# Performance work log

Measured on AMD Instinct MI355X. Metric: run time of the kernel, lower is better.

## Reference

```python
import jax, jax.numpy as jnp
import numpy as np

B, C, H, Wd = 16, 512, 56, 56
WCH = 128  # W_ch: projection rank of phi/rou


def setup_inputs() -> dict:
    key = jax.random.key(0)
    ks = jax.random.split(key, 8)
    s = 0.02
    return {
        "x": jax.random.normal(ks[0], (B, C, H, Wd), dtype=jnp.float32),
        "y": jax.random.normal(ks[1], (B, C, H, Wd), dtype=jnp.float32),
        # phi: Conv2d(C, WCH, 1) -> weight [WCH, C], bias [WCH]
        "phi_w": jax.random.normal(ks[2], (WCH, C), dtype=jnp.float32) * s,
        "phi_b": jnp.zeros((WCH,), dtype=jnp.float32),
        # rou: Conv2d(C, WCH, 1) applied to globally pooled y -> acts as Linear
        "rou_w": jax.random.normal(ks[3], (WCH, C), dtype=jnp.float32) * s,
        "rou_b": jnp.zeros((WCH,), dtype=jnp.float32),
        # zeta: Linear(C, C)
        "zeta_w": jax.random.normal(ks[4], (C, C), dtype=jnp.float32) * s,
        "zeta_b": jnp.zeros((C,), dtype=jnp.float32),
    }


def reference(x, y, phi_w, phi_b, rou_w, rou_b, zeta_w, zeta_b):
    b, c, h, w = x.shape
    hw = h * w
    # phi_xT = relu(phi(x)).view(B, WCH, HW); phi_x = transpose -> [B, HW, WCH]
    phi_xT = jax.nn.relu(jnp.einsum('kc,bchw->bkhw', phi_w, x) + phi_b[None, :, None, None])
    phi_x = phi_xT.reshape(b, -1, hw).transpose(0, 2, 1)  # [B, HW, WCH]
    # rou_y = sigmoid(rou(global_avg_pool(y))) -> [B, WCH]
    pooled = y.mean(axis=(2, 3))  # [B, C]
    rou_y = jax.nn.sigmoid(pooled @ rou_w.T + rou_b)  # [B, WCH]
    # D_i = sum_j (phi_x diag(rou) phi_x^T)_{ij} = sum_k phi_x[i,k] rou[k] s[k]
    s = phi_x.sum(axis=1)  # [B, WCH], column sums
    D = jnp.einsum('bnk,bk,bk->bn', phi_x, rou_y, s)  # [B, HW]
    inv_sqrt = 1.0 / jnp.sqrt(D + 1e-8)
    P = phi_x * inv_sqrt[..., None]  # diag(D^-1/2) @ phi_x, [B, HW, WCH]
    # x.view(B, -1, C): raw row-major reshape of [B,C,H,W] (NOT a transpose)
    x_trans = x.reshape(b, hw, c)
    # LX = x_trans - P diag(rou) P^T x_trans, re-associated right-to-left
    t = jnp.einsum('bnk,bnc->bkc', P, x_trans)          # P^T x_trans, [B, WCH, C]
    LX = x_trans - jnp.einsum('bnk,bk,bkc->bnc', P, rou_y, t)
    # zeta Linear + dropout(eval: identity) + relu, residual add
    out = jax.nn.relu(LX @ zeta_w.T + zeta_b)
    return x + out.reshape(b, c, h, w)
```

## Files before the change

### kernel.cpp

```cpp
#include <hip/hip_runtime.h>
#include <math.h>

#define B_  16
#define C_  512
#define HW_ 3136
#define K_  128
#define CHW (C_ * HW_)

typedef __bf16 bf16x8_t __attribute__((ext_vector_type(8)));
typedef __bf16 bf16x4_t __attribute__((ext_vector_type(4)));
typedef __bf16 bf16x2_t __attribute__((ext_vector_type(2)));
typedef float floatx4  __attribute__((ext_vector_type(4)));

typedef const __attribute__((address_space(1))) void* gas_ptr;
typedef __attribute__((address_space(3))) void*       las_ptr;

__device__ __forceinline__ void stage128x64(const __bf16* __restrict__ base, long ld,
                                            int row0, int rowmax, int k0,
                                            __bf16* lds, int t) {
    int w = t >> 6;
    #pragma unroll
    for (int i = 0; i < 4; ++i) {
        int u = i * 256 + t;
        int m = u >> 3, slot = u & 7;
        int kg = slot ^ (m & 7);
        int r = row0 + m; if (r > rowmax) r = rowmax;
        const __bf16* g = base + (long)r * ld + (k0 + kg * 8);
        __bf16* l = lds + (size_t)(i * 256 + w * 64) * 8;
        __builtin_amdgcn_global_load_lds((gas_ptr)g, (las_ptr)l, 16, 0, 0);
    }
}

__device__ __forceinline__ void mma_step64(const char* As, const char* Bs,
                                           floatx4 acc[4][4], int aoff, int boff,
                                           int q, int lxor) {
    #pragma unroll
    for (int h = 0; h < 2; ++h) {
        int s = (((h * 4 + q) ^ lxor) << 4);
        bf16x8_t af[4], bf[4];
        #pragma unroll
        for (int i = 0; i < 4; ++i)
            af[i] = *(const bf16x8_t*)(As + aoff + i * 2048 + s);
        #pragma unroll
        for (int i = 0; i < 4; ++i)
            bf[i] = *(const bf16x8_t*)(Bs + boff + i * 2048 + s);
        #pragma unroll
        for (int mi = 0; mi < 4; ++mi)
            #pragma unroll
            for (int ni = 0; ni < 4; ++ni)
                acc[mi][ni] = __builtin_amdgcn_mfma_f32_16x16x32_bf16(af[mi], bf[ni], acc[mi][ni], 0, 0, 0);
    }
}


__global__ __launch_bounds__(256) void k_pool(const float* __restrict__ y,
                                              float* __restrict__ pooled) {
    int bc = blockIdx.x;
    const float* yp = y + (long)bc * HW_;
    float acc = 0.f;
    for (int n = threadIdx.x; n < HW_; n += 256) acc += yp[n];
    __shared__ float red[256];
    red[threadIdx.x] = acc;
    __syncthreads();
    for (int s = 128; s > 0; s >>= 1) {
        if (threadIdx.x < s) red[threadIdx.x] += red[threadIdx.x + s];
        __syncthreads();
    }
    if (threadIdx.x == 0) pooled[bc] = red[0] * (1.0f / HW_);
}

__global__ __launch_bounds__(128) void k_rou(const float* __restrict__ pooled,
                                             const float* __restrict__ rou_w,
                                             const float* __restrict__ rou_b,
                                             float* __restrict__ rou_y) {
    int b = blockIdx.x;
    int k = threadIdx.x;
    __shared__ float ps[C_];
    for (int c = threadIdx.x; c < C_; c += 128) ps[c] = pooled[b * C_ + c];
    __syncthreads();
    float acc = rou_b[k];
    for (int c = 0; c < C_; ++c) acc += ps[c] * rou_w[k * C_ + c];
    rou_y[b * K_ + k] = 1.0f / (1.0f + expf(-acc));
}

__global__ __launch_bounds__(256) void k_cast8(const float* __restrict__ a,
                                               __bf16* __restrict__ o) {
    long i = ((long)blockIdx.x * 256 + threadIdx.x) * 8;
    float4 v0 = *reinterpret_cast<const float4*>(a + i);
    float4 v1 = *reinterpret_cast<const float4*>(a + i + 4);
    bf16x8_t r;
    r[0] = (__bf16)v0.x; r[1] = (__bf16)v0.y; r[2] = (__bf16)v0.z; r[3] = (__bf16)v0.w;
    r[4] = (__bf16)v1.x; r[5] = (__bf16)v1.y; r[6] = (__bf16)v1.z; r[7] = (__bf16)v1.w;
    *reinterpret_cast<bf16x8_t*>(o + i) = r;
}

__global__ __launch_bounds__(256) void k_prep(const float* __restrict__ xf,
                                              __bf16* __restrict__ xbf2,
                                              __bf16* __restrict__ x1t) {
    int b = blockIdx.z, c0 = blockIdx.y * 64, n0 = blockIdx.x * 64;
    __shared__ float ld[64][65];
    int t = threadIdx.x, tn = t & 63, g = t >> 6;
    const float* xb = xf + (long)b * CHW;
    __bf16* fb = xbf2 + (long)b * CHW;
    #pragma unroll 4
    for (int r = 0; r < 16; ++r) {
        int c = c0 + g * 16 + r;
        float v = xb[(long)c * HW_ + n0 + tn];
        ld[g * 16 + r][tn] = v;
        fb[(long)c * HW_ + n0 + tn] = (__bf16)v;
    }
    __syncthreads();
    __bf16* ob = x1t + (long)b * CHW;
    #pragma unroll 4
    for (int r = 0; r < 16; ++r) {
        int n = n0 + g * 16 + r;
        ob[(long)n * C_ + c0 + tn] = (__bf16)ld[tn][g * 16 + r];
    }
}

__global__ __launch_bounds__(256) void k_tr2s(const __bf16* __restrict__ xbf2,
                                              const float* __restrict__ inv_s,
                                              __bf16* __restrict__ x2s) {
    int b = blockIdx.z, c0 = blockIdx.y * 64, n0 = blockIdx.x * 64;
    __shared__ float ld[64][65];
    int t = threadIdx.x, tc = t & 63, g = t >> 6;
    const __bf16* xb = xbf2 + (long)b * CHW;
    #pragma unroll 4
    for (int r = 0; r < 16; ++r) {
        int n = n0 + g * 16 + r;
        ld[g * 16 + r][tc] = (float)xb[(long)n * C_ + c0 + tc] * inv_s[b * HW_ + n];
    }
    __syncthreads();
    __bf16* ob = x2s + (long)b * CHW;
    #pragma unroll 4
    for (int r = 0; r < 16; ++r) {
        int c = c0 + g * 16 + r;
        ob[(long)c * HW_ + n0 + tc] = (__bf16)ld[tc][g * 16 + r];
    }
}


__global__ __launch_bounds__(256) void k_phi_m(const __bf16* __restrict__ x1t,
                                               const __bf16* __restrict__ pwbf,
                                               const float* __restrict__ phi_b,
                                               __bf16* __restrict__ phi_kn,
                                               __bf16* __restrict__ phi_nk,
                                               float* __restrict__ sbuf) {
    int b = blockIdx.y;
    int n0 = blockIdx.x * 128;
    __shared__ __bf16 As[8192];
    __shared__ __bf16 Bs[8192];
    int t = threadIdx.x, w = t >> 6, lane = t & 63;
    int lm = lane & 15, q = lane >> 4;
    int wrow = w >> 1, wcol = w & 1;
    floatx4 acc[4][4];
    #pragma unroll
    for (int i = 0; i < 4; ++i)
        #pragma unroll
        for (int j = 0; j < 4; ++j) acc[i][j] = (floatx4){0.f, 0.f, 0.f, 0.f};

    const __bf16* Bb = x1t + (long)b * CHW;
    int lxor = lm & 7;
    int aoff = (wrow * 64 + lm) * 128;
    int boff = (wcol * 64 + lm) * 128;

    for (int p0 = 0; p0 < C_; p0 += 64) {
        stage128x64(pwbf, C_, 0, K_ - 1, p0, As, t);
        stage128x64(Bb,   C_, n0, HW_ - 1, p0, Bs, t);
        __syncthreads();
        mma_step64((const char*)As, (const char*)Bs, acc, aoff, boff, q, lxor);
        __syncthreads();
    }
    #pragma unroll
    for (int mi = 0; mi < 4; ++mi) {
        int kb = wrow * 64 + mi * 16 + q * 4;
        float4 pb = *reinterpret_cast<const float4*>(phi_b + kb);
        float pbv[4] = {pb.x, pb.y, pb.z, pb.w};
        float sv[4] = {0.f, 0.f, 0.f, 0.f};
        #pragma unroll
        for (int ni = 0; ni < 4; ++ni) {
            int n = n0 + wcol * 64 + ni * 16 + lm;
            if (n < HW_) {
                bf16x4_t pack;
                #pragma unroll
                for (int r = 0; r < 4; ++r) {
                    float v = fmaxf(acc[mi][ni][r] + pbv[r], 0.f);
                    __bf16 vb = (__bf16)v;
                    phi_kn[((long)b * K_ + kb + r) * HW_ + n] = vb;
                    pack[r] = vb;
                    sv[r] += v;
                }
                *reinterpret_cast<bf16x4_t*>(phi_nk + ((long)b * HW_ + n) * K_ + kb) = pack;
            }
        }
        #pragma unroll
        for (int r = 0; r < 4; ++r) {
            float v = sv[r];
            v += __shfl_xor(v, 1, 64); v += __shfl_xor(v, 2, 64);
            v += __shfl_xor(v, 4, 64); v += __shfl_xor(v, 8, 64);
            if (lm == 0) atomicAdd(&sbuf[b * K_ + kb + r], v);
        }
    }
}

__global__ __launch_bounds__(256) void k_d2(__bf16* __restrict__ phi_nk,
                                            const float* __restrict__ rou_y,
                                            const float* __restrict__ s,
                                            float* __restrict__ inv_s) {
    int b = blockIdx.y;
    __shared__ float ws[K_];
    int t = threadIdx.x;
    if (t < K_) ws[t] = rou_y[b * K_ + t] * s[b * K_ + t];
    __syncthreads();
    int w = t >> 6, lane = t & 63;
    int n = blockIdx.x * 4 + w;
    __bf16* p = phi_nk + ((long)b * HW_ + n) * K_ + lane * 2;
    bf16x2_t v = *reinterpret_cast<bf16x2_t*>(p);
    float f0 = (float)v[0], f1 = (float)v[1];
    float d = f0 * ws[lane * 2] + f1 * ws[lane * 2 + 1];
    #pragma unroll
    for (int off = 32; off > 0; off >>= 1) d += __shfl_xor(d, off, 64);
    float inv = rsqrtf(d + 1e-8f);
    bf16x2_t o; o[0] = (__bf16)(f0 * inv); o[1] = (__bf16)(f1 * inv);
    *reinterpret_cast<bf16x2_t*>(p) = o;
    if (lane == 0) inv_s[b * HW_ + n] = inv;
}

__global__ __launch_bounds__(256) void k_t_m(const __bf16* __restrict__ phi_kn,
                                             const __bf16* __restrict__ x2s,
                                             float* __restrict__ t_f32) {
    int b = blockIdx.z;
    int c0 = blockIdx.x * 128;
    int nch = blockIdx.y;
    __shared__ __bf16 As[8192];
    __shared__ __bf16 Bs[8192];
    int t = threadIdx.x, w = t >> 6, lane = t & 63;
    int lm = lane & 15, q = lane >> 4;
    int wrow = w >> 1, wcol = w & 1;
    floatx4 acc[4][4];
    #pragma unroll
    for (int i = 0; i < 4; ++i)
        #pragma unroll
        for (int j = 0; j < 4; ++j) acc[i][j] = (floatx4){0.f, 0.f, 0.f, 0.f};

    const __bf16* Ab = phi_kn + (long)b * K_ * HW_;
    const __bf16* Bb = x2s + (long)b * CHW;
    int lxor = lm & 7;
    int aoff = (wrow * 64 + lm) * 128;
    int boff = (wcol * 64 + lm) * 128;

    int pstart = nch * 448;
    for (int p0 = pstart; p0 < pstart + 448; p0 += 64) {
        stage128x64(Ab, HW_, 0, K_ - 1, p0, As, t);
        stage128x64(Bb, HW_, c0, C_ - 1, p0, Bs, t);
        __syncthreads();
        mma_step64((const char*)As, (const char*)Bs, acc, aoff, boff, q, lxor);
        __syncthreads();
    }
    #pragma unroll
    for (int mi = 0; mi < 4; ++mi) {
        int kb = wrow * 64 + mi * 16 + q * 4;
        #pragma unroll
        for (int ni = 0; ni < 4; ++ni) {
            int c = c0 + wcol * 64 + ni * 16 + lm;
            #pragma unroll
            for (int r = 0; r < 4; ++r)
                atomicAdd(&t_f32[((long)b * K_ + kb + r) * C_ + c], acc[mi][ni][r]);
        }
    }
}

__global__ __launch_bounds__(256) void k_tz_m(const __bf16* __restrict__ zwbf,
                                              const __bf16* __restrict__ t_bf,
                                              const float* __restrict__ rou_y,
                                              __bf16* __restrict__ tzT) {
    int b = blockIdx.y;
    int c0 = blockIdx.x * 128;
    __shared__ __bf16 As[8192];
    __shared__ __bf16 Bs[8192];
    int t = threadIdx.x, w = t >> 6, lane = t & 63;
    int lm = lane & 15, q = lane >> 4;
    int wrow = w >> 1, wcol = w & 1;
    floatx4 acc[4][4];
    #pragma unroll
    for (int i = 0; i < 4; ++i)
        #pragma unroll
        for (int j = 0; j < 4; ++j) acc[i][j] = (floatx4){0.f, 0.f, 0.f, 0.f};

    const __bf16* Bb = t_bf + (long)b * K_ * C_;
    int lxor = lm & 7;
    int aoff = (wrow * 64 + lm) * 128;
    int boff = (wcol * 64 + lm) * 128;

    for (int p0 = 0; p0 < C_; p0 += 64) {
        stage128x64(zwbf, C_, c0, C_ - 1, p0, As, t);
        stage128x64(Bb,   C_, 0, K_ - 1, p0, Bs, t);
        __syncthreads();
        mma_step64((const char*)As, (const char*)Bs, acc, aoff, boff, q, lxor);
        __syncthreads();
    }
    #pragma unroll
    for (int mi = 0; mi < 4; ++mi) {
        int c = c0 + wrow * 64 + mi * 16 + q * 4;
        #pragma unroll
        for (int ni = 0; ni < 4; ++ni) {
            int k = wcol * 64 + ni * 16 + lm;
            float rk = rou_y[b * K_ + k];
            #pragma unroll
            for (int r = 0; r < 4; ++r)
                tzT[((long)b * C_ + c + r) * K_ + k] = (__bf16)(-rk * acc[mi][ni][r]);
        }
    }
}

__global__ __launch_bounds__(256) void k_out_m(const __bf16* __restrict__ xbf2,
                                               const __bf16* __restrict__ zwbf,
                                               const __bf16* __restrict__ pnk,
                                               const __bf16* __restrict__ tzT,
                                               const float* __restrict__ zeta_b,
                                               float* __restrict__ out) {
    int b = blockIdx.z;
    int n0 = blockIdx.y * 128;
    int c0 = blockIdx.x * 128;
    __shared__ __attribute__((aligned(16))) char smem[32768];
    __bf16* As = (__bf16*)smem;
    __bf16* Bs = (__bf16*)(smem + 16384);
    int t = threadIdx.x, w = t >> 6, lane = t & 63;
    int lm = lane & 15, q = lane >> 4;
    int wrow = w >> 1, wcol = w & 1;
    floatx4 acc[4][4];
    #pragma unroll
    for (int i = 0; i < 4; ++i)
        #pragma unroll
        for (int j = 0; j < 4; ++j) acc[i][j] = (floatx4){0.f, 0.f, 0.f, 0.f};

    int lxor = lm & 7;
    int aoff = (wrow * 64 + lm) * 128;
    int boff = (wcol * 64 + lm) * 128;

    const __bf16* A1 = xbf2 + (long)b * CHW;
    for (int p0 = 0; p0 < C_; p0 += 64) {
        stage128x64(A1,   C_, n0, HW_ - 1, p0, As, t);
        stage128x64(zwbf, C_, c0, C_ - 1, p0, Bs, t);
        __syncthreads();
        mma_step64((const char*)As, (const char*)Bs, acc, aoff, boff, q, lxor);
        __syncthreads();
    }
    const __bf16* A2 = pnk + (long)b * (long)HW_ * K_;
    const __bf16* B2 = tzT + (long)b * (long)C_ * K_;
    for (int p0 = 0; p0 < K_; p0 += 64) {
        stage128x64(A2, K_, n0, HW_ - 1, p0, As, t);
        stage128x64(B2, K_, c0, C_ - 1, p0, Bs, t);
        __syncthreads();
        mma_step64((const char*)As, (const char*)Bs, acc, aoff, boff, q, lxor);
        __syncthreads();
    }
    float* ep = (float*)smem;
    const __bf16* xres = xbf2 + (long)b * CHW;
    int lr = t >> 3, lc = (t & 7) * 16;
    #pragma unroll
    for (int ch = 0; ch < 4; ++ch) {
        __syncthreads();
        if (wrow == (ch >> 1)) {
            #pragma unroll
            for (int mm = 0; mm < 2; ++mm) {
                int mi = (ch & 1) * 2 + mm;
                #pragma unroll
                for (int ni = 0; ni < 4; ++ni)
                    #pragma unroll
                    for (int r = 0; r < 4; ++r)
                        ep[(mm * 16 + q * 4 + r) * 132 + wcol * 64 + ni * 16 + lm] = acc[mi][ni][r];
            }
        }
        __syncthreads();
        int n = n0 + ch * 32 + lr;
        if (n < HW_) {
            long rowbase = (long)n * C_ + c0 + lc;
            bf16x8_t x0 = *(const bf16x8_t*)(xres + rowbase);
            bf16x8_t x1 = *(const bf16x8_t*)(xres + rowbase + 8);
            float xv[16];
            #pragma unroll
            for (int j = 0; j < 8; ++j) { xv[j] = (float)x0[j]; xv[8 + j] = (float)x1[j]; }
            float* orow = out + (long)b * CHW + rowbase;
            #pragma unroll
            for (int jj = 0; jj < 4; ++jj) {
                float4 zb = *reinterpret_cast<const float4*>(zeta_b + c0 + lc + jj * 4);
                float4 e  = *reinterpret_cast<const float4*>(&ep[lr * 132 + lc + jj * 4]);
                float4 o;
                o.x = xv[jj * 4 + 0] + fmaxf(e.x + zb.x, 0.f);
                o.y = xv[jj * 4 + 1] + fmaxf(e.y + zb.y, 0.f);
                o.z = xv[jj * 4 + 2] + fmaxf(e.z + zb.z, 0.f);
                o.w = xv[jj * 4 + 3] + fmaxf(e.w + zb.w, 0.f);
                *reinterpret_cast<float4*>(orow + jj * 4) = o;
            }
        }
    }
}

extern "C" void kernel_launch(void* const* d_in, const int* in_sizes, int n_in,
                              void* d_out, int out_size, void* d_ws, size_t ws_size,
                              hipStream_t stream) {
    const float* x      = (const float*)d_in[0];
    const float* y      = (const float*)d_in[1];
    const float* phi_w  = (const float*)d_in[2];
    const float* phi_b  = (const float*)d_in[3];
    const float* rou_w  = (const float*)d_in[4];
    const float* rou_b  = (const float*)d_in[5];
    const float* zeta_w = (const float*)d_in[6];
    const float* zeta_b = (const float*)d_in[7];
    float* out = (float*)d_out;

    char* p = (char*)d_ws;
    __bf16* xbf2   = (__bf16*)p; p += (size_t)B_ * CHW * 2;
    __bf16* x1t    = (__bf16*)p; p += (size_t)B_ * CHW * 2;
    __bf16* phi_kn = (__bf16*)p; p += (size_t)B_ * K_ * HW_ * 2;
    __bf16* phi_nk = (__bf16*)p; p += (size_t)B_ * K_ * HW_ * 2;
    float*  t_f32  = (float*) p; p += (size_t)B_ * K_ * C_ * 4;
    __bf16* tzT    = (__bf16*)p; p += (size_t)B_ * C_ * K_ * 2;
    __bf16* pwbf   = (__bf16*)p; p += (size_t)K_ * C_ * 2;
    __bf16* zwbf   = (__bf16*)p; p += (size_t)C_ * C_ * 2;
    float*  pooled = (float*) p; p += (size_t)B_ * C_ * 4;
    float*  rou_y  = (float*) p; p += (size_t)B_ * K_ * 4;
    float*  sbuf   = (float*) p; p += (size_t)B_ * K_ * 4;
    float*  inv_s  = (float*) p; p += (size_t)B_ * HW_ * 4;
    __bf16* x2s    = x1t;
    __bf16* t_bf   = x1t;

    hipMemsetAsync(sbuf, 0, B_ * K_ * sizeof(float), stream);
    hipMemsetAsync(t_f32, 0, (size_t)B_ * K_ * C_ * sizeof(float), stream);

    k_pool <<<B_ * C_, 256, 0, stream>>>(y, pooled);
    k_rou  <<<B_, 128, 0, stream>>>(pooled, rou_w, rou_b, rou_y);
    k_cast8<<<(K_ * C_) / 2048, 256, 0, stream>>>(phi_w, pwbf);
    k_cast8<<<(C_ * C_) / 2048, 256, 0, stream>>>(zeta_w, zwbf);
    k_prep <<<dim3(HW_ / 64, C_ / 64, B_), 256, 0, stream>>>(x, xbf2, x1t);
    k_phi_m<<<dim3(25, B_), 256, 0, stream>>>(x1t, pwbf, phi_b, phi_kn, phi_nk, sbuf);
    k_d2   <<<dim3(HW_ / 4, B_), 256, 0, stream>>>(phi_nk, rou_y, sbuf, inv_s);
    k_tr2s <<<dim3(HW_ / 64, C_ / 64, B_), 256, 0, stream>>>(xbf2, inv_s, x2s);
    k_t_m  <<<dim3(C_ / 128, 7, B_), 256, 0, stream>>>(phi_kn, x2s, t_f32);
    k_cast8<<<(B_ * K_ * C_) / 2048, 256, 0, stream>>>(t_f32, t_bf);
    k_tz_m <<<dim3(C_ / 128, B_), 256, 0, stream>>>(zwbf, t_bf, rou_y, tzT);
    k_out_m<<<dim3(C_ / 128, 25, B_), 256, 0, stream>>>(xbf2, zwbf, phi_nk, tzT, zeta_b, out);
}
```

Baseline: 476.3 us.

## Fuse transposes into GEMM staging and replace atomic split-K with partial reduction

Removes the separate transpose kernels (k_prep, k_tr2s). The phi and t GEMMs now read the raw bf16 copy of x and transpose it in-register while staging into a padded, swizzled LDS tile, with the inv_sqrt scaling folded into the t staging. Split-K atomics into t_f32, along with its memset, are replaced by per-chunk partial buffers reduced by a new kernel that also does the bf16 cast. Block indices of the t and out GEMMs are remapped to a 1D grid, which changes the order in which tiles are scheduled. This saves full-tensor transpose traffic and atomics, at the cost of synchronous global loads in place of async global_load_lds for the B operand, plus extra workspace for the partials.

```diff
diff --git a/kernel.cpp b/kernel.cpp
--- a/kernel.cpp
+++ b/kernel.cpp
@@ -14,6 +14,10 @@
 
 typedef const __attribute__((address_space(1))) void* gas_ptr;
 typedef __attribute__((address_space(3))) void*       las_ptr;
+
+static __device__ __forceinline__ unsigned short bfbits(__bf16 v) {
+    return __builtin_bit_cast(unsigned short, v);
+}
 
 __device__ __forceinline__ void stage128x64(const __bf16* __restrict__ base, long ld,
                                             int row0, int rowmax, int k0,
@@ -31,6 +35,53 @@
     }
 }
 
+__device__ __forceinline__ void stage_tr_phi(const __bf16* __restrict__ src,
+                                             int n0, int p0, char* Bs, int t) {
+    int ng = t & 15;
+    int cp2 = (t >> 4) * 2;
+    #pragma unroll
+    for (int ci = 0; ci < 2; ++ci) {
+        int cc = cp2 + ci * 32;
+        const __bf16* g0 = src + (long)(p0 + cc) * HW_ + n0 + ng * 8;
+        bf16x8_t v0 = *(const bf16x8_t*)g0;
+        bf16x8_t v1 = *(const bf16x8_t*)(g0 + HW_);
+        int r8 = cc >> 3, sub = (cc & 7) >> 1;
+        #pragma unroll
+        for (int j = 0; j < 8; ++j) {
+            int row = ng * 8 + j;
+            int slot = (r8 + row + (row >> 3)) & 7;
+            unsigned int pr = ((unsigned int)bfbits(v1[j]) << 16) | bfbits(v0[j]);
+            *(unsigned int*)(Bs + row * 144 + slot * 16 + sub * 4) = pr;
+        }
+    }
+}
+
+__device__ __forceinline__ void stage_tr_t(const __bf16* __restrict__ src,
+                                           const float* __restrict__ isrc,
+                                           int c0, int p0, char* Bs, int t) {
+    int cg = t & 15;
+    int np2 = (t >> 4) * 2;
+    #pragma unroll
+    for (int ni = 0; ni < 2; ++ni) {
+        int nn = np2 + ni * 32;
+        int n = p0 + nn;
+        float s0 = isrc[n], s1 = isrc[n + 1];
+        const __bf16* g0 = src + (long)n * C_ + c0 + cg * 8;
+        bf16x8_t v0 = *(const bf16x8_t*)g0;
+        bf16x8_t v1 = *(const bf16x8_t*)(g0 + C_);
+        int r8 = nn >> 3, sub = (nn & 7) >> 1;
+        #pragma unroll
+        for (int j = 0; j < 8; ++j) {
+            int row = cg * 8 + j;
+            int slot = (r8 + row + (row >> 3)) & 7;
+            __bf16 a0 = (__bf16)((float)v0[j] * s0);
+            __bf16 a1 = (__bf16)((float)v1[j] * s1);
+            unsigned int pr = ((unsigned int)bfbits(a1) << 16) | bfbits(a0);
+            *(unsigned int*)(Bs + row * 144 + slot * 16 + sub * 4) = pr;
+        }
+    }
+}
+
 __device__ __forceinline__ void mma_step64(const char* As, const char* Bs,
                                            floatx4 acc[4][4], int aoff, int boff,
                                            int q, int lxor) {
@@ -39,11 +90,35 @@
         int s = (((h * 4 + q) ^ lxor) << 4);
         bf16x8_t af[4], bf[4];
         #pragma unroll
-        for (int i = 0; i < 4; ++i)
-            af[i] = *(const bf16x8_t*)(As + aoff + i * 2048 + s);
-        #pragma unroll
-        for (int i = 0; i < 4; ++i)
-            bf[i] = *(const bf16x8_t*)(Bs + boff + i * 2048 + s);
+        for (int i = 0; i < 4; ++i) af[i] = *(const bf16x8_t*)(As + aoff + i * 2048 + s);
+        #pragma unroll
+        for (int i = 0; i < 4; ++i) bf[i] = *(const bf16x8_t*)(Bs + boff + i * 2048 + s);
+        #pragma unroll
+        for (int mi = 0; mi < 4; ++mi)
+            #pragma unroll
+            for (int ni = 0; ni < 4; ++ni)
+                acc[mi][ni] = __builtin_amdgcn_mfma_f32_16x16x32_bf16(af[mi], bf[ni], acc[mi][ni], 0, 0, 0);
+    }
+}
+
+__device__ __forceinline__ void mma_step_mix(const char* As, const char* Bs,
+                                             floatx4 acc[4][4], int lm, int q,
+                                             int wrow, int wcol) {
+    int lxor = lm & 7;
+    int aoff = (wrow * 64 + lm) * 128;
+    #pragma unroll
+    for (int h = 0; h < 2; ++h) {
+        int g = h * 4 + q;
+        int sa = (g ^ lxor) << 4;
+        bf16x8_t af[4], bf[4];
+        #pragma unroll
+        for (int i = 0; i < 4; ++i) af[i] = *(const bf16x8_t*)(As + aoff + i * 2048 + sa);
+        #pragma unroll
+        for (int i = 0; i < 4; ++i) {
+            int brow = wcol * 64 + i * 16 + lm;
+            int slot = (g + brow + (brow >> 3)) & 7;
+            bf[i] = *(const bf16x8_t*)(Bs + brow * 144 + slot * 16);
+        }
         #pragma unroll
         for (int mi = 0; mi < 4; ++mi)
             #pragma unroll
@@ -94,53 +169,8 @@
     *reinterpret_cast<bf16x8_t*>(o + i) = r;
 }
 
-__global__ __launch_bounds__(256) void k_prep(const float* __restrict__ xf,
-                                              __bf16* __restrict__ xbf2,
-                                              __bf16* __restrict__ x1t) {
-    int b = blockIdx.z, c0 = blockIdx.y * 64, n0 = blockIdx.x * 64;
-    __shared__ float ld[64][65];
-    int t = threadIdx.x, tn = t & 63, g = t >> 6;
-    const float* xb = xf + (long)b * CHW;
-    __bf16* fb = xbf2 + (long)b * CHW;
-    #pragma unroll 4
-    for (int r = 0; r < 16; ++r) {
-        int c = c0 + g * 16 + r;
-        float v = xb[(long)c * HW_ + n0 + tn];
-        ld[g * 16 + r][tn] = v;
-        fb[(long)c * HW_ + n0 + tn] = (__bf16)v;
-    }
-    __syncthreads();
-    __bf16* ob = x1t + (long)b * CHW;
-    #pragma unroll 4
-    for (int r = 0; r < 16; ++r) {
-        int n = n0 + g * 16 + r;
-        ob[(long)n * C_ + c0 + tn] = (__bf16)ld[tn][g * 16 + r];
-    }
-}
-
-__global__ __launch_bounds__(256) void k_tr2s(const __bf16* __restrict__ xbf2,
-                                              const float* __restrict__ inv_s,
-                                              __bf16* __restrict__ x2s) {
-    int b = blockIdx.z, c0 = blockIdx.y * 64, n0 = blockIdx.x * 64;
-    __shared__ float ld[64][65];
-    int t = threadIdx.x, tc = t & 63, g = t >> 6;
-    const __bf16* xb = xbf2 + (long)b * CHW;
-    #pragma unroll 4
-    for (int r = 0; r < 16; ++r) {
-        int n = n0 + g * 16 + r;
-        ld[g * 16 + r][tc] = (float)xb[(long)n * C_ + c0 + tc] * inv_s[b * HW_ + n];
-    }
-    __syncthreads();
-    __bf16* ob = x2s + (long)b * CHW;
-    #pragma unroll 4
-    for (int r = 0; r < 16; ++r) {
-        int c = c0 + g * 16 + r;
-        ob[(long)c * HW_ + n0 + tc] = (__bf16)ld[tc][g * 16 + r];
-    }
-}
-
-
-__global__ __launch_bounds__(256) void k_phi_m(const __bf16* __restrict__ x1t,
+
+__global__ __launch_bounds__(256) void k_phi_m(const __bf16* __restrict__ xbf2,
                                                const __bf16* __restrict__ pwbf,
                                                const float* __restrict__ phi_b,
                                                __bf16* __restrict__ phi_kn,
@@ -148,8 +178,8 @@
                                                float* __restrict__ sbuf) {
     int b = blockIdx.y;
     int n0 = blockIdx.x * 128;
-    __shared__ __bf16 As[8192];
-    __shared__ __bf16 Bs[8192];
+    __shared__ __attribute__((aligned(16))) char smem[16384 + 18432];
+    char* As = smem; char* Bs = smem + 16384;
     int t = threadIdx.x, w = t >> 6, lane = t & 63;
     int lm = lane & 15, q = lane >> 4;
     int wrow = w >> 1, wcol = w & 1;
@@ -159,16 +189,12 @@
         #pragma unroll
         for (int j = 0; j < 4; ++j) acc[i][j] = (floatx4){0.f, 0.f, 0.f, 0.f};
 
-    const __bf16* Bb = x1t + (long)b * CHW;
-    int lxor = lm & 7;
-    int aoff = (wrow * 64 + lm) * 128;
-    int boff = (wcol * 64 + lm) * 128;
-
+    const __bf16* Bb = xbf2 + (long)b * CHW;
     for (int p0 = 0; p0 < C_; p0 += 64) {
-        stage128x64(pwbf, C_, 0, K_ - 1, p0, As, t);
-        stage128x64(Bb,   C_, n0, HW_ - 1, p0, Bs, t);
-        __syncthreads();
-        mma_step64((const char*)As, (const char*)Bs, acc, aoff, boff, q, lxor);
+        stage128x64(pwbf, C_, 0, K_ - 1, p0, (__bf16*)As, t);
+        stage_tr_phi(Bb, n0, p0, Bs, t);
+        __syncthreads();
+        mma_step_mix(As, Bs, acc, lm, q, wrow, wcol);
         __syncthreads();
     }
     #pragma unroll
@@ -227,13 +253,16 @@
 }
 
 __global__ __launch_bounds__(256) void k_t_m(const __bf16* __restrict__ phi_kn,
-                                             const __bf16* __restrict__ x2s,
-                                             float* __restrict__ t_f32) {
-    int b = blockIdx.z;
-    int c0 = blockIdx.x * 128;
-    int nch = blockIdx.y;
-    __shared__ __bf16 As[8192];
-    __shared__ __bf16 Bs[8192];
+                                             const __bf16* __restrict__ xbf2,
+                                             const float* __restrict__ inv_s,
+                                             float* __restrict__ t_part) {
+    int gid = blockIdx.x;
+    int rlo = gid & 7, cc4 = (gid >> 3) & 3, r8 = gid >> 5;
+    int r = r8 * 8 + rlo;
+    int b = r / 7, nch = r % 7;
+    int c0 = cc4 * 128;
+    __shared__ __attribute__((aligned(16))) char smem[16384 + 18432];
+    char* As = smem; char* Bs = smem + 16384;
     int t = threadIdx.x, w = t >> 6, lane = t & 63;
     int lm = lane & 15, q = lane >> 4;
     int wrow = w >> 1, wcol = w & 1;
@@ -244,19 +273,18 @@
         for (int j = 0; j < 4; ++j) acc[i][j] = (floatx4){0.f, 0.f, 0.f, 0.f};
 
     const __bf16* Ab = phi_kn + (long)b * K_ * HW_;
-    const __bf16* Bb = x2s + (long)b * CHW;
-    int lxor = lm & 7;
-    int aoff = (wrow * 64 + lm) * 128;
-    int boff = (wcol * 64 + lm) * 128;
+    const __bf16* Bb = xbf2 + (long)b * CHW;
+    const float* ib = inv_s + (long)b * HW_;
 
     int pstart = nch * 448;
     for (int p0 = pstart; p0 < pstart + 448; p0 += 64) {
-        stage128x64(Ab, HW_, 0, K_ - 1, p0, As, t);
-        stage128x64(Bb, HW_, c0, C_ - 1, p0, Bs, t);
-        __syncthreads();
-        mma_step64((const char*)As, (const char*)Bs, acc, aoff, boff, q, lxor);
-        __syncthreads();
-    }
+        stage128x64(Ab, HW_, 0, K_ - 1, p0, (__bf16*)As, t);
+        stage_tr_t(Bb, ib, c0, p0, Bs, t);
+        __syncthreads();
+        mma_step_mix(As, Bs, acc, lm, q, wrow, wcol);
+        __syncthreads();
+    }
+    float* outp = t_part + ((long)nch * B_ + b) * K_ * C_;
     #pragma unroll
     for (int mi = 0; mi < 4; ++mi) {
         int kb = wrow * 64 + mi * 16 + q * 4;
@@ -264,10 +292,25 @@
         for (int ni = 0; ni < 4; ++ni) {
             int c = c0 + wcol * 64 + ni * 16 + lm;
             #pragma unroll
-            for (int r = 0; r < 4; ++r)
-                atomicAdd(&t_f32[((long)b * K_ + kb + r) * C_ + c], acc[mi][ni][r]);
-        }
-    }
+            for (int rr = 0; rr < 4; ++rr)
+                outp[(long)(kb + rr) * C_ + c] = acc[mi][ni][rr];
+        }
+    }
+}
+
+__global__ __launch_bounds__(256) void k_tred(const float* __restrict__ t_part,
+                                              __bf16* __restrict__ t_bf) {
+    const long BKC = (long)B_ * K_ * C_;
+    long i = ((long)blockIdx.x * 256 + threadIdx.x) * 4;
+    float4 s = *reinterpret_cast<const float4*>(t_part + i);
+    #pragma unroll
+    for (int p = 1; p < 7; ++p) {
+        float4 v = *reinterpret_cast<const float4*>(t_part + p * BKC + i);
+        s.x += v.x; s.y += v.y; s.z += v.z; s.w += v.w;
+    }
+    bf16x4_t o;
+    o[0] = (__bf16)s.x; o[1] = (__bf16)s.y; o[2] = (__bf16)s.z; o[3] = (__bf16)s.w;
+    *reinterpret_cast<bf16x4_t*>(t_bf + i) = o;
 }
 
 __global__ __launch_bounds__(256) void k_tz_m(const __bf16* __restrict__ zwbf,
@@ -276,8 +319,8 @@
                                               __bf16* __restrict__ tzT) {
     int b = blockIdx.y;
     int c0 = blockIdx.x * 128;
-    __shared__ __bf16 As[8192];
-    __shared__ __bf16 Bs[8192];
+    __shared__ __attribute__((aligned(16))) char smem[32768];
+    char* As = smem; char* Bs = smem + 16384;
     int t = threadIdx.x, w = t >> 6, lane = t & 63;
     int lm = lane & 15, q = lane >> 4;
     int wrow = w >> 1, wcol = w & 1;
@@ -293,10 +336,10 @@
     int boff = (wcol * 64 + lm) * 128;
 
     for (int p0 = 0; p0 < C_; p0 += 64) {
-        stage128x64(zwbf, C_, c0, C_ - 1, p0, As, t);
-        stage128x64(Bb,   C_, 0, K_ - 1, p0, Bs, t);
-        __syncthreads();
-        mma_step64((const char*)As, (const char*)Bs, acc, aoff, boff, q, lxor);
+        stage128x64(zwbf, C_, c0, C_ - 1, p0, (__bf16*)As, t);
+        stage128x64(Bb,   C_, 0, K_ - 1, p0, (__bf16*)Bs, t);
+        __syncthreads();
+        mma_step64(As, Bs, acc, aoff, boff, q, lxor);
         __syncthreads();
     }
     #pragma unroll
@@ -307,8 +350,8 @@
             int k = wcol * 64 + ni * 16 + lm;
             float rk = rou_y[b * K_ + k];
             #pragma unroll
-            for (int r = 0; r < 4; ++r)
-                tzT[((long)b * C_ + c + r) * K_ + k] = (__bf16)(-rk * acc[mi][ni][r]);
+            for (int rr = 0; rr < 4; ++rr)
+                tzT[((long)b * C_ + c + rr) * K_ + k] = (__bf16)(-rk * acc[mi][ni][rr]);
         }
     }
 }
@@ -319,12 +362,14 @@
                                                const __bf16* __restrict__ tzT,
                                                const float* __restrict__ zeta_b,
                                                float* __restrict__ out) {
-    int b = blockIdx.z;
-    int n0 = blockIdx.y * 128;
-    int c0 = blockIdx.x * 128;
+    int gid = blockIdx.x;
+    int rlo = gid & 7, cc4 = (gid >> 3) & 3, r8 = gid >> 5;
+    int r = r8 * 8 + rlo;
+    int b = r / 25, nt = r % 25;
+    int n0 = nt * 128;
+    int c0 = cc4 * 128;
     __shared__ __attribute__((aligned(16))) char smem[32768];
-    __bf16* As = (__bf16*)smem;
-    __bf16* Bs = (__bf16*)(smem + 16384);
+    char* As = smem; char* Bs = smem + 16384;
     int t = threadIdx.x, w = t >> 6, lane = t & 63;
     int lm = lane & 15, q = lane >> 4;
     int wrow = w >> 1, wcol = w & 1;
@@ -340,19 +385,19 @@
 
     const __bf16* A1 = xbf2 + (long)b * CHW;
     for (int p0 = 0; p0 < C_; p0 += 64) {
-        stage128x64(A1,   C_, n0, HW_ - 1, p0, As, t);
-        stage128x64(zwbf, C_, c0, C_ - 1, p0, Bs, t);
-        __syncthreads();
-        mma_step64((const char*)As, (const char*)Bs, acc, aoff, boff, q, lxor);
+        stage128x64(A1,   C_, n0, HW_ - 1, p0, (__bf16*)As, t);
+        stage128x64(zwbf, C_, c0, C_ - 1, p0, (__bf16*)Bs, t);
+        __syncthreads();
+        mma_step64(As, Bs, acc, aoff, boff, q, lxor);
         __syncthreads();
     }
     const __bf16* A2 = pnk + (long)b * (long)HW_ * K_;
     const __bf16* B2 = tzT + (long)b * (long)C_ * K_;
     for (int p0 = 0; p0 < K_; p0 += 64) {
-        stage128x64(A2, K_, n0, HW_ - 1, p0, As, t);
-        stage128x64(B2, K_, c0, C_ - 1, p0, Bs, t);
-        __syncthreads();
-        mma_step64((const char*)As, (const char*)Bs, acc, aoff, boff, q, lxor);
+        stage128x64(A2, K_, n0, HW_ - 1, p0, (__bf16*)As, t);
+        stage128x64(B2, K_, c0, C_ - 1, p0, (__bf16*)Bs, t);
+        __syncthreads();
+        mma_step64(As, Bs, acc, aoff, boff, q, lxor);
         __syncthreads();
     }
     float* ep = (float*)smem;
@@ -368,8 +413,8 @@
                 #pragma unroll
                 for (int ni = 0; ni < 4; ++ni)
                     #pragma unroll
-                    for (int r = 0; r < 4; ++r)
-                        ep[(mm * 16 + q * 4 + r) * 132 + wcol * 64 + ni * 16 + lm] = acc[mi][ni][r];
+                    for (int rr = 0; rr < 4; ++rr)
+                        ep[(mm * 16 + q * 4 + rr) * 132 + wcol * 64 + ni * 16 + lm] = acc[mi][ni][rr];
             }
         }
         __syncthreads();
@@ -412,10 +457,10 @@
 
     char* p = (char*)d_ws;
     __bf16* xbf2   = (__bf16*)p; p += (size_t)B_ * CHW * 2;
-    __bf16* x1t    = (__bf16*)p; p += (size_t)B_ * CHW * 2;
     __bf16* phi_kn = (__bf16*)p; p += (size_t)B_ * K_ * HW_ * 2;
     __bf16* phi_nk = (__bf16*)p; p += (size_t)B_ * K_ * HW_ * 2;
-    float*  t_f32  = (float*) p; p += (size_t)B_ * K_ * C_ * 4;
+    float*  t_part = (float*) p; p += (size_t)7 * B_ * K_ * C_ * 4;
+    __bf16* t_bf   = (__bf16*)p; p += (size_t)B_ * K_ * C_ * 2;
     __bf16* tzT    = (__bf16*)p; p += (size_t)B_ * C_ * K_ * 2;
     __bf16* pwbf   = (__bf16*)p; p += (size_t)K_ * C_ * 2;
     __bf16* zwbf   = (__bf16*)p; p += (size_t)C_ * C_ * 2;
@@ -423,22 +468,18 @@
     float*  rou_y  = (float*) p; p += (size_t)B_ * K_ * 4;
     float*  sbuf   = (float*) p; p += (size_t)B_ * K_ * 4;
     float*  inv_s  = (float*) p; p += (size_t)B_ * HW_ * 4;
-    __bf16* x2s    = x1t;
-    __bf16* t_bf   = x1t;
 
     hipMemsetAsync(sbuf, 0, B_ * K_ * sizeof(float), stream);
-    hipMemsetAsync(t_f32, 0, (size_t)B_ * K_ * C_ * sizeof(float), stream);
 
     k_pool <<<B_ * C_, 256, 0, stream>>>(y, pooled);
     k_rou  <<<B_, 128, 0, stream>>>(pooled, rou_w, rou_b, rou_y);
     k_cast8<<<(K_ * C_) / 2048, 256, 0, stream>>>(phi_w, pwbf);
     k_cast8<<<(C_ * C_) / 2048, 256, 0, stream>>>(zeta_w, zwbf);
-    k_prep <<<dim3(HW_ / 64, C_ / 64, B_), 256, 0, stream>>>(x, xbf2, x1t);
-    k_phi_m<<<dim3(25, B_), 256, 0, stream>>>(x1t, pwbf, phi_b, phi_kn, phi_nk, sbuf);
+    k_cast8<<<(B_ * (long)CHW) / 2048, 256, 0, stream>>>(x, xbf2);
+    k_phi_m<<<dim3(25, B_), 256, 0, stream>>>(xbf2, pwbf, phi_b, phi_kn, phi_nk, sbuf);
     k_d2   <<<dim3(HW_ / 4, B_), 256, 0, stream>>>(phi_nk, rou_y, sbuf, inv_s);
-    k_tr2s <<<dim3(HW_ / 64, C_ / 64, B_), 256, 0, stream>>>(xbf2, inv_s, x2s);
-    k_t_m  <<<dim3(C_ / 128, 7, B_), 256, 0, stream>>>(phi_kn, x2s, t_f32);
-    k_cast8<<<(B_ * K_ * C_) / 2048, 256, 0, stream>>>(t_f32, t_bf);
+    k_t_m  <<<448, 256, 0, stream>>>(phi_kn, xbf2, inv_s, t_part);
+    k_tred <<<(B_ * K_ * C_) / 1024, 256, 0, stream>>>(t_part, t_bf);
     k_tz_m <<<dim3(C_ / 128, B_), 256, 0, stream>>>(zwbf, t_bf, rou_y, tzT);
-    k_out_m<<<dim3(C_ / 128, 25, B_), 256, 0, stream>>>(xbf2, zwbf, phi_nk, tzT, zeta_b, out);
-}
+    k_out_m<<<1600, 256, 0, stream>>>(xbf2, zwbf, phi_nk, tzT, zeta_b, out);
+}
```

Measured after the change: 428.0 us. -10.1%, faster.
